# Performance work log

Measured on AMD Instinct MI355X. Metric: run time of the kernel, lower is better.

Reference implementation:

```python
import jax, jax.numpy as jnp
import numpy as np

N = 50000
E = 1600000
IN_CH = 128
HID = 32
HEADS = 4
OUT_CH = 64
NEG_SLOPE = 0.2


def _seg_softmax(e, seg, n):
    # e: [E,H], seg: [E] destination indices -> per-destination softmax
    m = jax.ops.segment_max(e, seg, num_segments=n)          # [N,H]
    ex = jnp.exp(e - m[seg])
    s = jax.ops.segment_sum(ex, seg, num_segments=n)         # [N,H]
    return ex / (s[seg] + 1e-16)


def _gat_conv(x, edge_index, W, a_src, a_dst, b, concat):
    # x: [N,Fin]; W: [Fin, H*C]; a_src/a_dst: [H,C]; b: [H*C] or [C]
    H, C = a_src.shape
    n = x.shape[0]
    h = (x @ W).reshape(n, H, C)                              # [N,H,C]
    src, dst = edge_index[0], edge_index[1]
    as_ = jnp.einsum('nhc,hc->nh', h, a_src)                  # [N,H]
    ad_ = jnp.einsum('nhc,hc->nh', h, a_dst)
    e = jax.nn.leaky_relu(as_[src] + ad_[dst], NEG_SLOPE)     # [E,H]
    alpha = _seg_softmax(e, dst, n)                           # [E,H]
    msg = h[src] * alpha[:, :, None]                          # [E,H,C]
    out = jax.ops.segment_sum(msg, dst, num_segments=n)       # [N,H,C]
    out = out.reshape(n, H * C) if concat else out.mean(axis=1)
    return out + b, alpha


def _layer_norm(x, w, b, eps=1e-5):
    mu = x.mean(-1, keepdims=True)
    var = x.var(-1, keepdims=True)
    return (x - mu) * jax.lax.rsqrt(var + eps) * w + b


def setup_inputs() -> dict:
    key = jax.random.key(0)
    ks = jax.random.split(key, 20)
    g = lambda k, s: jax.random.normal(k, s, dtype=jnp.float32) * 0.05
    d = {
        'x': jax.random.normal(ks[0], (N, IN_CH), dtype=jnp.float32),
        'edge_index': jax.random.randint(ks[1], (2, E), 0, N, dtype=jnp.int64),
        # gat1: in=IN_CH, out=HID, heads, concat
        'W1': g(ks[2], (IN_CH, HEADS * HID)),
        'a_src1': g(ks[3], (HEADS, HID)),
        'a_dst1': g(ks[4], (HEADS, HID)),
        'b1': jnp.zeros((HEADS * HID,), jnp.float32),
        'ln1_w': jnp.ones((HEADS * HID,), jnp.float32),
        'ln1_b': jnp.zeros((HEADS * HID,), jnp.float32),
        'Wskip': g(ks[5], (IN_CH, HEADS * HID)),
        'bskip': jnp.zeros((HEADS * HID,), jnp.float32),
        # gat2: in=HEADS*HID, out=HID, concat
        'W2': g(ks[6], (HEADS * HID, HEADS * HID)),
        'a_src2': g(ks[7], (HEADS, HID)),
        'a_dst2': g(ks[8], (HEADS, HID)),
        'b2': jnp.zeros((HEADS * HID,), jnp.float32),
        'ln2_w': jnp.ones((HEADS * HID,), jnp.float32),
        'ln2_b': jnp.zeros((HEADS * HID,), jnp.float32),
        # gat3: in=HEADS*HID, out=OUT_CH, concat=False (mean over heads)
        'W3': g(ks[9], (HEADS * HID, HEADS * OUT_CH)),
        'a_src3': g(ks[10], (HEADS, OUT_CH)),
        'a_dst3': g(ks[11], (HEADS, OUT_CH)),
        'b3': jnp.zeros((OUT_CH,), jnp.float32),
    }
    return d


def reference(x, edge_index, W1, a_src1, a_dst1, b1, ln1_w, ln1_b,
              Wskip, bskip, W2, a_src2, a_dst2, b2, ln2_w, ln2_b,
              W3, a_src3, a_dst3, b3):
    x_skip = x
    h, alpha1 = _gat_conv(x, edge_index, W1, a_src1, a_dst1, b1, concat=True)
    h = jax.nn.elu(h)
    h = _layer_norm(h, ln1_w, ln1_b)
    h = h + (x_skip @ Wskip + bskip)
    h, alpha2 = _gat_conv(h, edge_index, W2, a_src2, a_dst2, b2, concat=True)
    h = jax.nn.elu(h)
    h = _layer_norm(h, ln2_w, ln2_b)
    out, alpha3 = _gat_conv(h, edge_index, W3, a_src3, a_dst3, b3, concat=False)
    return out, alpha1, alpha2, alpha3
```

## Files before the change

kernel.cpp:

```cpp
#include <hip/hip_runtime.h>

#define NN 50000
#define EE 1600000
#define SCAN_B 196
#define NB 196
#define CHUNK 2048
#define G1 782
#define L1 (NB * G1)
#define B1 599

typedef __attribute__((ext_vector_type(8))) short bf16x8;
typedef __attribute__((ext_vector_type(4))) float f32x4;

__device__ __forceinline__ float bfu(unsigned short u) { return __uint_as_float((unsigned)u << 16); }
__device__ __forceinline__ float bflo(unsigned u) { return __uint_as_float(u << 16); }
__device__ __forceinline__ float bfhi(unsigned u) { return __uint_as_float(u & 0xffff0000u); }
__device__ __forceinline__ unsigned short f2bf(float f) {
    unsigned u = __float_as_uint(f);
    u += 0x7fff + ((u >> 16) & 1);
    return (unsigned short)(u >> 16);
}
__device__ __forceinline__ unsigned pk2(float a, float b) {
    return (unsigned)f2bf(a) | ((unsigned)f2bf(b) << 16);
}
__device__ __forceinline__ float cvt_load(const void* p, int i, bool f32) {
    if (f32) return ((const float*)p)[i];
    return bfu(((const unsigned short*)p)[i]);
}

__global__ void detect_k(const void* ei_raw, const void* x_raw, int* flags) {
    __shared__ int s_i64, s_f32;
    const int t = threadIdx.x;
    if (t == 0) { s_i64 = 1; s_f32 = 0; }
    __syncthreads();
    const int* ei32 = (const int*)ei_raw;
    if (ei32[2 * t + 1] != 0) atomicAnd(&s_i64, 0);
    const unsigned short* xu = (const unsigned short*)x_raw;
    int found = 0;
    for (int j = 0; j < 32; j++) {
        unsigned short u = xu[t * 32 + j];
        if ((u & 0x7F80) == 0x7F80) found = 1;
    }
    if (found) atomicOr(&s_f32, 1);
    __syncthreads();
    if (t == 0) { flags[0] = s_i64; flags[1] = s_f32; }
}

__global__ __launch_bounds__(256) void hist1_k(const void* ei_raw, const int* flags,
                                               int2* __restrict__ edges, int* __restrict__ cnt)
{
    __shared__ int h[NB];
    const int t = threadIdx.x;
    const int i64 = __builtin_amdgcn_readfirstlane(flags[0]);
    if (t < NB) h[t] = 0;
    __syncthreads();
    const int beg = blockIdx.x * CHUNK;
    const int end = min(beg + CHUNK, EE);
    for (int e = beg + t; e < end; e += 256) {
        int2 v;
        if (i64) { const long long* p = (const long long*)ei_raw; v.x = (int)p[e]; v.y = (int)p[EE + e]; }
        else     { const int* p = (const int*)ei_raw;             v.x = p[e];      v.y = p[EE + e];      }
        edges[e] = v;
        atomicAdd(&h[v.y >> 8], 1);
    }
    __syncthreads();
    if (t < NB) cnt[(size_t)t * G1 + blockIdx.x] = h[t];
}

__global__ __launch_bounds__(256) void scanAg_k(int* __restrict__ cnt, int* __restrict__ bsum2) {
    __shared__ int ps[256];
    const int b = blockIdx.x, t = threadIdx.x;
    const int i = b * 256 + t;
    const int v = (i < L1) ? cnt[i] : 0;
    ps[t] = v;
    __syncthreads();
    for (int off = 1; off < 256; off <<= 1) {
        const int u = (t >= off) ? ps[t - off] : 0;
        __syncthreads();
        ps[t] += u;
        __syncthreads();
    }
    if (i < L1) cnt[i] = ps[t] - v;
    if (t == 255) bsum2[b] = ps[255];
}
__global__ void scanBg_k(int* bsum2) {
    __shared__ int ps[256];
    const int t = threadIdx.x;
    int vals[3];
    int s = 0;
    #pragma unroll
    for (int i = 0; i < 3; i++) {
        const int idx = t * 3 + i;
        vals[i] = (idx < B1) ? bsum2[idx] : 0;
        s += vals[i];
    }
    ps[t] = s;
    __syncthreads();
    for (int off = 1; off < 256; off <<= 1) {
        const int u = (t >= off) ? ps[t - off] : 0;
        __syncthreads();
        ps[t] += u;
        __syncthreads();
    }
    int run = t ? ps[t - 1] : 0;
    #pragma unroll
    for (int i = 0; i < 3; i++) {
        const int idx = t * 3 + i;
        if (idx < B1) bsum2[idx] = run;
        run += vals[i];
    }
}
__global__ __launch_bounds__(256) void scanCg_k(int* __restrict__ cnt, const int* __restrict__ bsum2,
                                                int* __restrict__ bstart) {
    const int i = blockIdx.x * 256 + threadIdx.x;
    if (i < L1) {
        const int r = cnt[i] + bsum2[blockIdx.x];
        cnt[i] = r;
        if (i % G1 == 0) bstart[i / G1] = r;
    }
    if (i == 0) bstart[NB] = EE;
}

__global__ __launch_bounds__(256) void scatter_k(const int2* __restrict__ edges,
                                                 const int* __restrict__ cnt,
                                                 int2* __restrict__ bedges)
{
    __shared__ int ofs[NB];
    const int t = threadIdx.x;
    if (t < NB) ofs[t] = cnt[(size_t)t * G1 + blockIdx.x];
    __syncthreads();
    const int beg = blockIdx.x * CHUNK;
    const int end = min(beg + CHUNK, EE);
    for (int e = beg + t; e < end; e += 256) {
        const int2 v = edges[e];
        const int p = atomicAdd(&ofs[v.y >> 8], 1);
        bedges[p] = v;
    }
}

__global__ __launch_bounds__(256) void hist_k(const int2* __restrict__ bedges,
                                              const int* __restrict__ bstart, int* __restrict__ deg)
{
    __shared__ int h[256];
    const int b = blockIdx.x, t = threadIdx.x;
    h[t] = 0;
    __syncthreads();
    const int lo = bstart[b], hi = bstart[b + 1];
    for (int i = lo + t; i < hi; i += 256)
        atomicAdd(&h[bedges[i].y & 255], 1);
    __syncthreads();
    const int d = b * 256 + t;
    if (d < NN) deg[d] = h[t];
}

__global__ __launch_bounds__(256) void scanA_k(const int* __restrict__ deg,
                                               int* __restrict__ roff, int* __restrict__ bsum) {
    __shared__ int ps[256];
    const int b = blockIdx.x, t = threadIdx.x;
    const int i = b * 256 + t;
    const int v = (i < NN) ? deg[i] : 0;
    ps[t] = v;
    __syncthreads();
    for (int off = 1; off < 256; off <<= 1) {
        const int u = (t >= off) ? ps[t - off] : 0;
        __syncthreads();
        ps[t] += u;
        __syncthreads();
    }
    if (i < NN) roff[i] = ps[t] - v;
    if (t == 255) bsum[b] = ps[255];
}
__global__ void scanB_k(int* bsum) {
    __shared__ int ps[256];
    const int t = threadIdx.x;
    const int v = (t < SCAN_B) ? bsum[t] : 0;
    ps[t] = v;
    __syncthreads();
    for (int off = 1; off < 256; off <<= 1) {
        const int u = (t >= off) ? ps[t - off] : 0;
        __syncthreads();
        ps[t] += u;
        __syncthreads();
    }
    if (t < SCAN_B) bsum[t] = ps[t] - v;
}
__global__ __launch_bounds__(256) void scanC_k(int* __restrict__ roff, const int* __restrict__ bsum) {
    const int b = blockIdx.x, t = threadIdx.x;
    const int i = b * 256 + t;
    if (i < NN) roff[i] += bsum[b];
}

__global__ __launch_bounds__(256) void place_k(const int2* __restrict__ bedges,
                                               const int* __restrict__ bstart, const int* __restrict__ roff,
                                               int* __restrict__ csrc)
{
    __shared__ int cur[256];
    const int b = blockIdx.x, t = threadIdx.x;
    const int d = b * 256 + t;
    cur[t] = (d < NN) ? roff[d] : 0;
    __syncthreads();
    const int lo = bstart[b], hi = bstart[b + 1];
    for (int i = lo + t; i < hi; i += 256) {
        const int2 v = bedges[i];
        const int p = atomicAdd(&cur[v.y & 255], 1);
        csrc[p] = v.x;
    }
}

__global__ __launch_bounds__(256) void cvt_all_k(
    const void* x, const void* W1, const void* Wskip, const void* W2, const void* W3,
    const void* as1, const void* ad1, const void* b1, const void* l1w, const void* l1b,
    const void* bsk, const void* as2, const void* ad2, const void* b2, const void* l2w,
    const void* l2b, const void* as3, const void* ad3, const void* b3,
    unsigned short* xb, unsigned short* Wt1, unsigned short* Wts, unsigned short* Wt2,
    unsigned short* Wt3, float* smalls, const int* flags)
{
    const bool f32 = __builtin_amdgcn_readfirstlane(flags[1]) != 0;
    const int gid = blockIdx.x * 256 + threadIdx.x;
    if (gid < NN * 128) { xb[gid] = f2bf(cvt_load(x, gid, f32)); return; }
    int g = gid - NN * 128;
    if (g < 16384) { Wt1[g] = f2bf(cvt_load(W1,    (g & 127) * 128 + (g >> 7), f32)); return; }
    g -= 16384;
    if (g < 16384) { Wts[g] = f2bf(cvt_load(Wskip, (g & 127) * 128 + (g >> 7), f32)); return; }
    g -= 16384;
    if (g < 16384) { Wt2[g] = f2bf(cvt_load(W2,    (g & 127) * 128 + (g >> 7), f32)); return; }
    g -= 16384;
    if (g < 32768) { Wt3[g] = f2bf(cvt_load(W3,    (g & 127) * 256 + (g >> 7), f32)); return; }
    g -= 32768;
    if (g >= 2432) return;
    const void* src; int off;
    if      (g < 128)  { src = as1; off = g;        }
    else if (g < 256)  { src = ad1; off = g - 128;  }
    else if (g < 384)  { src = b1;  off = g - 256;  }
    else if (g < 512)  { src = l1w; off = g - 384;  }
    else if (g < 640)  { src = l1b; off = g - 512;  }
    else if (g < 768)  { src = bsk; off = g - 640;  }
    else if (g < 896)  { src = as2; off = g - 768;  }
    else if (g < 1024) { src = ad2; off = g - 896;  }
    else if (g < 1152) { src = b2;  off = g - 1024; }
    else if (g < 1280) { src = l2w; off = g - 1152; }
    else if (g < 1408) { src = l2b; off = g - 1280; }
    else if (g < 1664) { src = as3; off = g - 1408; }
    else if (g < 1920) { src = ad3; off = g - 1664; }
    else               { src = b3;  off = g - 1920; }
    smalls[g] = cvt_load(src, off, f32);
}

__global__ void prep_v_k(const unsigned short* __restrict__ Wt3, const float* __restrict__ as3,
                         const float* __restrict__ ad3, float* __restrict__ vsrc, float* __restrict__ vdst)
{
    const int t = blockIdx.x * 256 + threadIdx.x;
    if (t >= 512) return;
    const int h = t >> 7, k = t & 127;
    float ss = 0.f, dd = 0.f;
    for (int c = 0; c < 64; c++) {
        const float w = bfu(Wt3[(size_t)(h * 64 + c) * 128 + k]);
        ss = fmaf(w, as3[h * 64 + c], ss);
        dd = fmaf(w, ad3[h * 64 + c], dd);
    }
    vsrc[t] = ss; vdst[t] = dd;
}

template<int FOUT>
__global__ __launch_bounds__(256) void mfma_mm_k(
    const unsigned short* __restrict__ Xb, const unsigned short* __restrict__ Wt,
    unsigned short* __restrict__ Hb)
{
    constexpr int NT = FOUT / 16;
    const int tile = blockIdx.x * 4 + (threadIdx.x >> 6);
    if (tile >= 3125) return;
    const int l = threadIdx.x & 63;
    const int lr = l & 15, lq = l >> 4;
    const int m0 = tile * 16;
    f32x4 acc[NT];
    #pragma unroll
    for (int nt = 0; nt < NT; nt++) { acc[nt][0]=0.f; acc[nt][1]=0.f; acc[nt][2]=0.f; acc[nt][3]=0.f; }
    #pragma unroll
    for (int kb = 0; kb < 4; kb++) {
        const bf16x8 a = *(const bf16x8*)(Xb + (size_t)(m0 + lr) * 128 + kb * 32 + lq * 8);
        #pragma unroll
        for (int nt = 0; nt < NT; nt++) {
            const bf16x8 b = *(const bf16x8*)(Wt + (size_t)(nt * 16 + lr) * 128 + kb * 32 + lq * 8);
            acc[nt] = __builtin_amdgcn_mfma_f32_16x16x32_bf16(a, b, acc[nt], 0, 0, 0);
        }
    }
    #pragma unroll
    for (int nt = 0; nt < NT; nt++)
        #pragma unroll
        for (int r = 0; r < 4; r++)
            Hb[(size_t)(m0 + lq * 4 + r) * FOUT + nt * 16 + lr] = f2bf(acc[nt][r]);
}

__global__ __launch_bounds__(256) void mm12_k(
    const unsigned short* __restrict__ Xb, const unsigned short* __restrict__ Wt1,
    unsigned short* __restrict__ Hb, unsigned short* __restrict__ Sb)
{
    const int tile = blockIdx.x * 4 + (threadIdx.x >> 6);
    if (tile >= 3125) return;
    const int l = threadIdx.x & 63;
    const int lr = l & 15, lq = l >> 4;
    const int m0 = tile * 16;
    f32x4 acc[16];
    #pragma unroll
    for (int nt = 0; nt < 16; nt++) { acc[nt][0]=0.f; acc[nt][1]=0.f; acc[nt][2]=0.f; acc[nt][3]=0.f; }
    #pragma unroll
    for (int kb = 0; kb < 4; kb++) {
        const bf16x8 a = *(const bf16x8*)(Xb + (size_t)(m0 + lr) * 128 + kb * 32 + lq * 8);
        #pragma unroll
        for (int nt = 0; nt < 16; nt++) {
            const bf16x8 b = *(const bf16x8*)(Wt1 + (size_t)(nt * 16 + lr) * 128 + kb * 32 + lq * 8);
            acc[nt] = __builtin_amdgcn_mfma_f32_16x16x32_bf16(a, b, acc[nt], 0, 0, 0);
        }
    }
    #pragma unroll
    for (int nt = 0; nt < 8; nt++)
        #pragma unroll
        for (int r = 0; r < 4; r++)
            Hb[(size_t)(m0 + lq * 4 + r) * 128 + nt * 16 + lr] = f2bf(acc[nt][r]);
    #pragma unroll
    for (int nt = 8; nt < 16; nt++)
        #pragma unroll
        for (int r = 0; r < 4; r++)
            Sb[(size_t)(m0 + lq * 4 + r) * 128 + (nt - 8) * 16 + lr] = f2bf(acc[nt][r]);
}

__global__ __launch_bounds__(256) void dots_k(
    const unsigned short* __restrict__ Hb, const float* __restrict__ asrc,
    const float* __restrict__ adst, float* __restrict__ as_, float* __restrict__ dpk)
{
    const int node = blockIdx.x * 4 + (threadIdx.x >> 6);
    const int l = threadIdx.x & 63;
    const unsigned hv = *(const unsigned*)(Hb + (size_t)node * 128 + 2 * l);
    const float h0 = bfu((unsigned short)hv), h1 = bfu((unsigned short)(hv >> 16));
    const int hd = l >> 4;
    const int cc = (2 * l) & 31;
    float ps = h0 * asrc[hd * 32 + cc] + h1 * asrc[hd * 32 + cc + 1];
    float pd = h0 * adst[hd * 32 + cc] + h1 * adst[hd * 32 + cc + 1];
    #pragma unroll
    for (int m = 8; m; m >>= 1) { ps += __shfl_xor(ps, m); pd += __shfl_xor(pd, m); }
    if ((l & 15) == 0) {
        as_[(size_t)node * 4 + hd] = ps;
        dpk[(size_t)node * 8 + hd] = pd;
    }
}

__global__ __launch_bounds__(256) void dots3_k(
    const unsigned short* __restrict__ Xb, const float* __restrict__ vsrc,
    const float* __restrict__ vdst, float* __restrict__ as_, float* __restrict__ dpk)
{
    const int node = blockIdx.x * 4 + (threadIdx.x >> 6);
    const int l = threadIdx.x & 63;
    const unsigned hv = *(const unsigned*)(Xb + (size_t)node * 128 + 2 * l);
    const float x0 = bfu((unsigned short)hv), x1 = bfu((unsigned short)(hv >> 16));
    float s[4], d[4];
    #pragma unroll
    for (int h = 0; h < 4; h++) {
        s[h] = x0 * vsrc[h * 128 + 2 * l] + x1 * vsrc[h * 128 + 2 * l + 1];
        d[h] = x0 * vdst[h * 128 + 2 * l] + x1 * vdst[h * 128 + 2 * l + 1];
    }
    #pragma unroll
    for (int m = 32; m; m >>= 1)
        #pragma unroll
        for (int h = 0; h < 4; h++) { s[h] += __shfl_xor(s[h], m); d[h] += __shfl_xor(d[h], m); }
    if (l == 0) {
        #pragma unroll
        for (int h = 0; h < 4; h++) {
            as_[(size_t)node * 4 + h] = s[h];
            dpk[(size_t)node * 8 + h] = d[h];
        }
    }
}

__device__ __forceinline__ float4 edge_w(float4 as4, float4 ad4) {
    float4 e4;
    e4.x = as4.x + ad4.x; e4.y = as4.y + ad4.y; e4.z = as4.z + ad4.z; e4.w = as4.w + ad4.w;
    e4.x = e4.x >= 0.f ? e4.x : 0.2f * e4.x;
    e4.y = e4.y >= 0.f ? e4.y : 0.2f * e4.y;
    e4.z = e4.z >= 0.f ? e4.z : 0.2f * e4.z;
    e4.w = e4.w >= 0.f ? e4.w : 0.2f * e4.w;
    float4 w4;
    w4.x = __expf(e4.x); w4.y = __expf(e4.y); w4.z = __expf(e4.z); w4.w = __expf(e4.w);
    return w4;
}

template<bool HAS_SKIP>
__global__ __launch_bounds__(256) void fagg12_k(
    const int* __restrict__ roff, const int* __restrict__ deg,
    const int* __restrict__ csrc, const float* __restrict__ as_, float* __restrict__ dpk,
    const unsigned short* __restrict__ Hb,
    const float* __restrict__ b, const float* __restrict__ lnw, const float* __restrict__ lnb,
    const unsigned short* __restrict__ skipb, const float* __restrict__ bskip,
    unsigned short* __restrict__ xoutb)
{
    __shared__ float lws[4][512];
    const int warp = threadIdx.x >> 6;
    const int lane = threadIdx.x & 63;
    const int node = blockIdx.x * 4 + warp;
    const int q = lane & 15, g = lane >> 4;
    const int h = q >> 2;
    float* lw = lws[warp];
    const int ro = roff[node], dg = deg[node];
    const float4 ad4 = *(const float4*)(dpk + (size_t)node * 8);

    float4 sv = make_float4(0.f, 0.f, 0.f, 0.f);
    float acc[8];
    #pragma unroll
    for (int i = 0; i < 8; i++) acc[i] = 0.f;

    for (int j0 = 0; j0 < dg; j0 += 64) {
        const int jn = min(64, dg - j0);
        int src = 0;
        float4 w4 = make_float4(0.f, 0.f, 0.f, 0.f);
        if (lane < jn) {
            src = csrc[ro + j0 + lane];
            const float4 as4 = *(const float4*)(as_ + (size_t)src * 4);
            w4 = edge_w(as4, ad4);
            sv.x += w4.x; sv.y += w4.y; sv.z += w4.z; sv.w += w4.w;
        }
        const float sf = __int_as_float(src);
        *(float4*)(lw + lane * 8)     = make_float4(w4.x, sf, w4.y, sf);
        *(float4*)(lw + lane * 8 + 4) = make_float4(w4.z, sf, w4.w, sf);
        const int jq = (jn + 3) >> 2;
        #pragma unroll 2
        for (int j = 0; j < jq; j++) {
            const int e = 4 * j + g;
            const float2 rd = *(const float2*)(lw + e * 8 + h * 2);
            const float w = rd.x;
            const unsigned soff = (__float_as_uint(rd.y) << 8) + (unsigned)(q << 4);
            const uint4 hv = *(const uint4*)((const char*)Hb + soff);
            acc[0] = fmaf(w, bflo(hv.x), acc[0]);
            acc[1] = fmaf(w, bfhi(hv.x), acc[1]);
            acc[2] = fmaf(w, bflo(hv.y), acc[2]);
            acc[3] = fmaf(w, bfhi(hv.y), acc[3]);
            acc[4] = fmaf(w, bflo(hv.z), acc[4]);
            acc[5] = fmaf(w, bfhi(hv.z), acc[5]);
            acc[6] = fmaf(w, bflo(hv.w), acc[6]);
            acc[7] = fmaf(w, bfhi(hv.w), acc[7]);
        }
    }

    #pragma unroll
    for (int i = 0; i < 8; i++) {
        acc[i] += __shfl_xor(acc[i], 16);
        acc[i] += __shfl_xor(acc[i], 32);
    }
    #pragma unroll
    for (int m = 32; m; m >>= 1) {
        sv.x += __shfl_xor(sv.x, m); sv.y += __shfl_xor(sv.y, m);
        sv.z += __shfl_xor(sv.z, m); sv.w += __shfl_xor(sv.w, m);
    }
    float4 rs;
    rs.x = 1.f / (sv.x + 1e-16f); rs.y = 1.f / (sv.y + 1e-16f);
    rs.z = 1.f / (sv.z + 1e-16f); rs.w = 1.f / (sv.w + 1e-16f);
    if (lane == 0) *(float4*)(dpk + (size_t)node * 8 + 4) = rs;
    const float rsh = (h == 0) ? rs.x : (h == 1) ? rs.y : (h == 2) ? rs.z : rs.w;

    const float4 b0 = *(const float4*)(b + q * 8);
    const float4 b1 = *(const float4*)(b + q * 8 + 4);
    float v[8];
    v[0] = acc[0] * rsh + b0.x; v[1] = acc[1] * rsh + b0.y;
    v[2] = acc[2] * rsh + b0.z; v[3] = acc[3] * rsh + b0.w;
    v[4] = acc[4] * rsh + b1.x; v[5] = acc[5] * rsh + b1.y;
    v[6] = acc[6] * rsh + b1.z; v[7] = acc[7] * rsh + b1.w;
    float s1 = 0.f, s2 = 0.f;
    #pragma unroll
    for (int i = 0; i < 8; i++) {
        v[i] = v[i] > 0.f ? v[i] : expm1f(v[i]);
        s1 += v[i]; s2 += v[i] * v[i];
    }
    #pragma unroll
    for (int m = 8; m; m >>= 1) { s1 += __shfl_xor(s1, m); s2 += __shfl_xor(s2, m); }
    const float mu   = s1 * (1.f / 128.f);
    const float var  = s2 * (1.f / 128.f) - mu * mu;
    const float rstd = rsqrtf(var + 1e-5f);
    const float4 w0 = *(const float4*)(lnw + q * 8);
    const float4 w1 = *(const float4*)(lnw + q * 8 + 4);
    const float4 o0 = *(const float4*)(lnb + q * 8);
    const float4 o1 = *(const float4*)(lnb + q * 8 + 4);
    float y[8];
    y[0] = (v[0] - mu) * rstd * w0.x + o0.x; y[1] = (v[1] - mu) * rstd * w0.y + o0.y;
    y[2] = (v[2] - mu) * rstd * w0.z + o0.z; y[3] = (v[3] - mu) * rstd * w0.w + o0.w;
    y[4] = (v[4] - mu) * rstd * w1.x + o1.x; y[5] = (v[5] - mu) * rstd * w1.y + o1.y;
    y[6] = (v[6] - mu) * rstd * w1.z + o1.z; y[7] = (v[7] - mu) * rstd * w1.w + o1.w;
    if (HAS_SKIP) {
        const uint4 sk = *(const uint4*)(skipb + (size_t)node * 128 + q * 8);
        const float4 k0 = *(const float4*)(bskip + q * 8);
        const float4 k1 = *(const float4*)(bskip + q * 8 + 4);
        y[0] += bflo(sk.x) + k0.x; y[1] += bfhi(sk.x) + k0.y;
        y[2] += bflo(sk.y) + k0.z; y[3] += bfhi(sk.y) + k0.w;
        y[4] += bflo(sk.z) + k1.x; y[5] += bfhi(sk.z) + k1.y;
        y[6] += bflo(sk.w) + k1.z; y[7] += bfhi(sk.w) + k1.w;
    }
    if (g == 0) {
        uint4 pk;
        pk.x = pk2(y[0], y[1]); pk.y = pk2(y[2], y[3]);
        pk.z = pk2(y[4], y[5]); pk.w = pk2(y[6], y[7]);
        *(uint4*)(xoutb + (size_t)node * 128 + q * 8) = pk;
    }
}

__global__ __launch_bounds__(256) void fagg3_k(
    const int* __restrict__ roff, const int* __restrict__ deg,
    const int* __restrict__ csrc, const float* __restrict__ as_, float* __restrict__ dpk,
    const unsigned short* __restrict__ Xb,
    unsigned short* __restrict__ gout)
{
    __shared__ float lws[4][256];
    __shared__ int lss[4][64];
    const int warp = threadIdx.x >> 6;
    const int lane = threadIdx.x & 63;
    const int node = blockIdx.x * 4 + warp;
    const int q = lane & 31, g = lane >> 5;
    float* lw = lws[warp];
    int*   ls = lss[warp];
    const int ro = roff[node], dg = deg[node];
    const float4 ad4 = *(const float4*)(dpk + (size_t)node * 8);

    float4 sv = make_float4(0.f, 0.f, 0.f, 0.f);
    float acc[4][4];
    #pragma unroll
    for (int hh = 0; hh < 4; hh++)
        #pragma unroll
        for (int i = 0; i < 4; i++) acc[hh][i] = 0.f;

    for (int j0 = 0; j0 < dg; j0 += 64) {
        const int jn = min(64, dg - j0);
        int src = 0;
        float4 w4 = make_float4(0.f, 0.f, 0.f, 0.f);
        if (lane < jn) {
            src = csrc[ro + j0 + lane];
            const float4 as4 = *(const float4*)(as_ + (size_t)src * 4);
            w4 = edge_w(as4, ad4);
            sv.x += w4.x; sv.y += w4.y; sv.z += w4.z; sv.w += w4.w;
        }
        *(float4*)(lw + lane * 4) = w4;
        ls[lane] = src;
        const int jq = (jn + 1) >> 1;
        #pragma unroll 2
        for (int j = 0; j < jq; j++) {
            const int e = 2 * j + g;
            const float4 w = *(const float4*)(lw + e * 4);
            const int s_ = ls[e];
            const unsigned soff = ((unsigned)s_ << 8) + (unsigned)(q << 3);
            const uint2 hv = *(const uint2*)((const char*)Xb + soff);
            const float x0 = bflo(hv.x), x1 = bfhi(hv.x);
            const float x2 = bflo(hv.y), x3 = bfhi(hv.y);
            acc[0][0] = fmaf(w.x, x0, acc[0][0]); acc[0][1] = fmaf(w.x, x1, acc[0][1]);
            acc[0][2] = fmaf(w.x, x2, acc[0][2]); acc[0][3] = fmaf(w.x, x3, acc[0][3]);
            acc[1][0] = fmaf(w.y, x0, acc[1][0]); acc[1][1] = fmaf(w.y, x1, acc[1][1]);
            acc[1][2] = fmaf(w.y, x2, acc[1][2]); acc[1][3] = fmaf(w.y, x3, acc[1][3]);
            acc[2][0] = fmaf(w.z, x0, acc[2][0]); acc[2][1] = fmaf(w.z, x1, acc[2][1]);
            acc[2][2] = fmaf(w.z, x2, acc[2][2]); acc[2][3] = fmaf(w.z, x3, acc[2][3]);
            acc[3][0] = fmaf(w.w, x0, acc[3][0]); acc[3][1] = fmaf(w.w, x1, acc[3][1]);
            acc[3][2] = fmaf(w.w, x2, acc[3][2]); acc[3][3] = fmaf(w.w, x3, acc[3][3]);
        }
    }

    #pragma unroll
    for (int hh = 0; hh < 4; hh++)
        #pragma unroll
        for (int i = 0; i < 4; i++) acc[hh][i] += __shfl_xor(acc[hh][i], 32);
    #pragma unroll
    for (int m = 32; m; m >>= 1) {
        sv.x += __shfl_xor(sv.x, m); sv.y += __shfl_xor(sv.y, m);
        sv.z += __shfl_xor(sv.z, m); sv.w += __shfl_xor(sv.w, m);
    }
    float4 rs;
    rs.x = 1.f / (sv.x + 1e-16f); rs.y = 1.f / (sv.y + 1e-16f);
    rs.z = 1.f / (sv.z + 1e-16f); rs.w = 1.f / (sv.w + 1e-16f);
    if (lane == 0) *(float4*)(dpk + (size_t)node * 8 + 4) = rs;

    unsigned short* gr = gout + (size_t)node * 512 + 4 * q;
    if (g == 0) {
        uint2 p0, p1;
        p0.x = pk2(acc[0][0] * rs.x, acc[0][1] * rs.x);
        p0.y = pk2(acc[0][2] * rs.x, acc[0][3] * rs.x);
        p1.x = pk2(acc[1][0] * rs.y, acc[1][1] * rs.y);
        p1.y = pk2(acc[1][2] * rs.y, acc[1][3] * rs.y);
        *(uint2*)(gr)       = p0;
        *(uint2*)(gr + 128) = p1;
    } else {
        uint2 p2, p3;
        p2.x = pk2(acc[2][0] * rs.z, acc[2][1] * rs.z);
        p2.y = pk2(acc[2][2] * rs.z, acc[2][3] * rs.z);
        p3.x = pk2(acc[3][0] * rs.w, acc[3][1] * rs.w);
        p3.y = pk2(acc[3][2] * rs.w, acc[3][3] * rs.w);
        *(uint2*)(gr + 256) = p2;
        *(uint2*)(gr + 384) = p3;
    }
}

__global__ __launch_bounds__(256) void alpha_l_k(
    const int2* __restrict__ edges, const float* __restrict__ as_,
    const float* __restrict__ dpk, float* __restrict__ al)
{
    const int e = blockIdx.x * 256 + threadIdx.x;
    const int2 v = edges[e];
    const float4 as4 = *(const float4*)(as_ + (size_t)v.x * 4);
    const float4 ad4 = *(const float4*)(dpk + (size_t)v.y * 8);
    const float4 r   = *(const float4*)(dpk + (size_t)v.y * 8 + 4);
    const float4 w = edge_w(as4, ad4);
    float4 a; a.x = w.x * r.x; a.y = w.y * r.y; a.z = w.z * r.z; a.w = w.w * r.w;
    *(float4*)(al + (size_t)e * 4) = a;
}

__global__ __launch_bounds__(256) void proj3_k(
    const unsigned short* __restrict__ Gb, const unsigned short* __restrict__ Wt3,
    const float* __restrict__ b3, float* __restrict__ out)
{
    const int tile = blockIdx.x * 4 + (threadIdx.x >> 6);
    if (tile >= 3125) return;
    const int l = threadIdx.x & 63;
    const int lr = l & 15, lq = l >> 4;
    const int m0 = tile * 16;
    f32x4 acc[4];
    #pragma unroll
    for (int nt = 0; nt < 4; nt++) { acc[nt][0]=0.f; acc[nt][1]=0.f; acc[nt][2]=0.f; acc[nt][3]=0.f; }
    #pragma unroll
    for (int kb = 0; kb < 16; kb++) {
        const int h = kb >> 2;
        const int kk = (kb & 3) * 32 + lq * 8;
        const bf16x8 a = *(const bf16x8*)(Gb + (size_t)(m0 + lr) * 512 + kb * 32 + lq * 8);
        #pragma unroll
        for (int nt = 0; nt < 4; nt++) {
            const int c = nt * 16 + lr;
            const bf16x8 b = *(const bf16x8*)(Wt3 + (size_t)(h * 64 + c) * 128 + kk);
            acc[nt] = __builtin_amdgcn_mfma_f32_16x16x32_bf16(a, b, acc[nt], 0, 0, 0);
        }
    }
    #pragma unroll
    for (int nt = 0; nt < 4; nt++)
        #pragma unroll
        for (int r = 0; r < 4; r++) {
            const int col = nt * 16 + lr;
            out[(size_t)(m0 + lq * 4 + r) * 64 + col] = 0.25f * acc[nt][r] + b3[col];
        }
}

extern "C" void kernel_launch(void* const* d_in, const int* in_sizes, int n_in,
                              void* d_out, int out_size, void* d_ws, size_t ws_size,
                              hipStream_t stream)
{
    char* ws = (char*)d_ws;
    unsigned short* g_bf    = (unsigned short*)(ws);
    int2*           bedges  = (int2*)(ws);
    int*            csrc    = (int*)(ws + 51200000);
    unsigned short* x_bf    = (unsigned short*)(ws + 57600000);
    unsigned short* xcur_bf = (unsigned short*)(ws + 70400000);
    unsigned short* skip_bf = (unsigned short*)(ws + 83200000);
    unsigned short* Hbuf    = (unsigned short*)(ws + 96000000);
    int2*  edges  = (int2*)(ws + 108800000);
    float* as1b   = (float*)(ws + 121600000);
    float* as2b   = as1b + 200000;
    float* as3b   = as1b + 400000;
    float* dpk1   = as1b + 600000;
    float* dpk2   = as1b + 1000000;
    float* dpk3   = as1b + 1400000;
    int*   roff   = (int*)(ws + 128800000);
    int*   deg    = (int*)(ws + 129000000);
    int*   bsum   = (int*)(ws + 129200000);
    int*   flags  = (int*)(ws + 129402048);
    unsigned short* Wt1 = (unsigned short*)(ws + 129500000);
    unsigned short* Wts = Wt1 + 16384;
    unsigned short* Wt2 = Wts + 16384;
    unsigned short* Wt3 = Wt2 + 16384;
    float* smalls = (float*)(ws + 129700000);
    float* vsrc   = (float*)(ws + 129720000);
    float* vdst   = (float*)(ws + 129730000);
    int*   cnt    = (int*)(ws + 130000000);
    int*   bsum2  = (int*)(ws + 130700000);
    int*   bstart = (int*)(ws + 130710000);

    float* as1c = smalls;          float* ad1c = smalls + 128;
    float* b1c  = smalls + 256;    float* l1wc = smalls + 384;
    float* l1bc = smalls + 512;    float* bskc = smalls + 640;
    float* as2c = smalls + 768;    float* ad2c = smalls + 896;
    float* b2c  = smalls + 1024;   float* l2wc = smalls + 1152;
    float* l2bc = smalls + 1280;   float* as3c = smalls + 1408;
    float* ad3c = smalls + 1664;   float* b3c  = smalls + 1920;

    float* out = (float*)d_out;
    float* al1 = out + (size_t)NN * 64;
    float* al2 = al1 + (size_t)EE * 4;
    float* al3 = al2 + (size_t)EE * 4;

    detect_k<<<1, 256, 0, stream>>>(d_in[1], d_in[0], flags);
    hist1_k<<<G1, 256, 0, stream>>>(d_in[1], flags, edges, cnt);
    cvt_all_k<<<25330, 256, 0, stream>>>(
        d_in[0], d_in[2], d_in[8], d_in[10], d_in[16],
        d_in[3], d_in[4], d_in[5], d_in[6], d_in[7],
        d_in[9], d_in[11], d_in[12], d_in[13], d_in[14], d_in[15],
        d_in[17], d_in[18], d_in[19],
        x_bf, Wt1, Wts, Wt2, Wt3, smalls, flags);
    scanAg_k<<<B1, 256, 0, stream>>>(cnt, bsum2);
    scanBg_k<<<1, 256, 0, stream>>>(bsum2);
    scanCg_k<<<B1, 256, 0, stream>>>(cnt, bsum2, bstart);
    scatter_k<<<G1, 256, 0, stream>>>(edges, cnt, bedges);
    hist_k<<<NB, 256, 0, stream>>>(bedges, bstart, deg);
    scanA_k<<<SCAN_B, 256, 0, stream>>>(deg, roff, bsum);
    scanB_k<<<1, 256, 0, stream>>>(bsum);
    scanC_k<<<SCAN_B, 256, 0, stream>>>(roff, bsum);
    place_k<<<NB, 256, 0, stream>>>(bedges, bstart, roff, csrc);
    prep_v_k<<<2, 256, 0, stream>>>(Wt3, as3c, ad3c, vsrc, vdst);

    mm12_k<<<782, 256, 0, stream>>>(x_bf, Wt1, Hbuf, skip_bf);
    dots_k<<<12500, 256, 0, stream>>>(Hbuf, as1c, ad1c, as1b, dpk1);
    fagg12_k<true><<<12500, 256, 0, stream>>>(roff, deg, csrc, as1b, dpk1, Hbuf,
                                              b1c, l1wc, l1bc, skip_bf, bskc, xcur_bf);

    mfma_mm_k<128><<<782, 256, 0, stream>>>(xcur_bf, Wt2, Hbuf);
    dots_k<<<12500, 256, 0, stream>>>(Hbuf, as2c, ad2c, as2b, dpk2);
    fagg12_k<false><<<12500, 256, 0, stream>>>(roff, deg, csrc, as2b, dpk2, Hbuf,
                                               b2c, l2wc, l2bc, nullptr, nullptr, xcur_bf);

    dots3_k<<<12500, 256, 0, stream>>>(xcur_bf, vsrc, vdst, as3b, dpk3);
    fagg3_k<<<12500, 256, 0, stream>>>(roff, deg, csrc, as3b, dpk3, xcur_bf, g_bf);
    proj3_k<<<782, 256, 0, stream>>>(g_bf, Wt3, b3c, out);

    alpha_l_k<<<6250, 256, 0, stream>>>(edges, as1b, dpk1, al1);
    alpha_l_k<<<6250, 256, 0, stream>>>(edges, as2b, dpk2, al2);
    alpha_l_k<<<6250, 256, 0, stream>>>(edges, as3b, dpk3, al3);
}
```

Baseline: 605.2 us.

## Fuse attention dot products into matmul and aggregation epilogues; use packed FMA

Removes the separate dots_k and dots3_k launches. The per-node source and destination attention scores are now computed in the epilogues of the MFMA matmul kernels, and for layer 3 in the fagg12 layer-2 epilogue from the fp32 LayerNorm output. The aggregation inner loops also switch to 2-wide float vectors with elementwise fma, to encourage packed FMA instructions. This saves three kernel launches and three re-reads of the hidden features. The cost is extra shuffles and registers in the matmul and aggregation kernels, and layer-3 scores come from fp32 rather than bf16-rounded values.

Result: faster. 580.2 us (-4.1%).

```diff
diff --git a/kernel.cpp b/kernel.cpp
--- a/kernel.cpp
+++ b/kernel.cpp
@@ -11,10 +11,20 @@
 
 typedef __attribute__((ext_vector_type(8))) short bf16x8;
 typedef __attribute__((ext_vector_type(4))) float f32x4;
+typedef __attribute__((ext_vector_type(2))) float f32x2;
+
+#if __has_builtin(__builtin_elementwise_fma)
+#define PKFMA(a, b, c) __builtin_elementwise_fma((a), (b), (c))
+#else
+#define PKFMA(a, b, c) ((a) * (b) + (c))
+#endif
 
 __device__ __forceinline__ float bfu(unsigned short u) { return __uint_as_float((unsigned)u << 16); }
 __device__ __forceinline__ float bflo(unsigned u) { return __uint_as_float(u << 16); }
 __device__ __forceinline__ float bfhi(unsigned u) { return __uint_as_float(u & 0xffff0000u); }
+__device__ __forceinline__ f32x2 bfpk(unsigned u) {
+    f32x2 r; r.x = bflo(u); r.y = bfhi(u); return r;
+}
 __device__ __forceinline__ unsigned short f2bf(float f) {
     unsigned u = __float_as_uint(f);
     u += 0x7fff + ((u >> 16) & 1);
@@ -261,10 +271,12 @@
     vsrc[t] = ss; vdst[t] = dd;
 }
 
-template<int FOUT>
+template<int FOUT, bool DOTS>
 __global__ __launch_bounds__(256) void mfma_mm_k(
     const unsigned short* __restrict__ Xb, const unsigned short* __restrict__ Wt,
-    unsigned short* __restrict__ Hb)
+    unsigned short* __restrict__ Hb,
+    const float* __restrict__ asrc, const float* __restrict__ adst,
+    float* __restrict__ as_, float* __restrict__ dpk)
 {
     constexpr int NT = FOUT / 16;
     const int tile = blockIdx.x * 4 + (threadIdx.x >> 6);
@@ -289,11 +301,32 @@
         #pragma unroll
         for (int r = 0; r < 4; r++)
             Hb[(size_t)(m0 + lq * 4 + r) * FOUT + nt * 16 + lr] = f2bf(acc[nt][r]);
+    if (DOTS) {
+        #pragma unroll
+        for (int hd = 0; hd < 4; hd++) {
+            const float a0 = asrc[hd * 32 + lr], a1 = asrc[hd * 32 + 16 + lr];
+            const float d0 = adst[hd * 32 + lr], d1 = adst[hd * 32 + 16 + lr];
+            #pragma unroll
+            for (int r = 0; r < 4; r++) {
+                float ps = acc[2 * hd][r] * a0 + acc[2 * hd + 1][r] * a1;
+                float pd = acc[2 * hd][r] * d0 + acc[2 * hd + 1][r] * d1;
+                #pragma unroll
+                for (int m = 8; m; m >>= 1) { ps += __shfl_xor(ps, m); pd += __shfl_xor(pd, m); }
+                if (lr == 0) {
+                    const int node = m0 + lq * 4 + r;
+                    as_[(size_t)node * 4 + hd] = ps;
+                    dpk[(size_t)node * 8 + hd] = pd;
+                }
+            }
+        }
+    }
 }
 
 __global__ __launch_bounds__(256) void mm12_k(
     const unsigned short* __restrict__ Xb, const unsigned short* __restrict__ Wt1,
-    unsigned short* __restrict__ Hb, unsigned short* __restrict__ Sb)
+    unsigned short* __restrict__ Hb, unsigned short* __restrict__ Sb,
+    const float* __restrict__ asrc, const float* __restrict__ adst,
+    float* __restrict__ as_, float* __restrict__ dpk)
 {
     const int tile = blockIdx.x * 4 + (threadIdx.x >> 6);
     if (tile >= 3125) return;
@@ -322,51 +355,21 @@
         #pragma unroll
         for (int r = 0; r < 4; r++)
             Sb[(size_t)(m0 + lq * 4 + r) * 128 + (nt - 8) * 16 + lr] = f2bf(acc[nt][r]);
-}
-
-__global__ __launch_bounds__(256) void dots_k(
-    const unsigned short* __restrict__ Hb, const float* __restrict__ asrc,
-    const float* __restrict__ adst, float* __restrict__ as_, float* __restrict__ dpk)
-{
-    const int node = blockIdx.x * 4 + (threadIdx.x >> 6);
-    const int l = threadIdx.x & 63;
-    const unsigned hv = *(const unsigned*)(Hb + (size_t)node * 128 + 2 * l);
-    const float h0 = bfu((unsigned short)hv), h1 = bfu((unsigned short)(hv >> 16));
-    const int hd = l >> 4;
-    const int cc = (2 * l) & 31;
-    float ps = h0 * asrc[hd * 32 + cc] + h1 * asrc[hd * 32 + cc + 1];
-    float pd = h0 * adst[hd * 32 + cc] + h1 * adst[hd * 32 + cc + 1];
-    #pragma unroll
-    for (int m = 8; m; m >>= 1) { ps += __shfl_xor(ps, m); pd += __shfl_xor(pd, m); }
-    if ((l & 15) == 0) {
-        as_[(size_t)node * 4 + hd] = ps;
-        dpk[(size_t)node * 8 + hd] = pd;
-    }
-}
-
-__global__ __launch_bounds__(256) void dots3_k(
-    const unsigned short* __restrict__ Xb, const float* __restrict__ vsrc,
-    const float* __restrict__ vdst, float* __restrict__ as_, float* __restrict__ dpk)
-{
-    const int node = blockIdx.x * 4 + (threadIdx.x >> 6);
-    const int l = threadIdx.x & 63;
-    const unsigned hv = *(const unsigned*)(Xb + (size_t)node * 128 + 2 * l);
-    const float x0 = bfu((unsigned short)hv), x1 = bfu((unsigned short)(hv >> 16));
-    float s[4], d[4];
-    #pragma unroll
-    for (int h = 0; h < 4; h++) {
-        s[h] = x0 * vsrc[h * 128 + 2 * l] + x1 * vsrc[h * 128 + 2 * l + 1];
-        d[h] = x0 * vdst[h * 128 + 2 * l] + x1 * vdst[h * 128 + 2 * l + 1];
-    }
-    #pragma unroll
-    for (int m = 32; m; m >>= 1)
-        #pragma unroll
-        for (int h = 0; h < 4; h++) { s[h] += __shfl_xor(s[h], m); d[h] += __shfl_xor(d[h], m); }
-    if (l == 0) {
-        #pragma unroll
-        for (int h = 0; h < 4; h++) {
-            as_[(size_t)node * 4 + h] = s[h];
-            dpk[(size_t)node * 8 + h] = d[h];
+    #pragma unroll
+    for (int hd = 0; hd < 4; hd++) {
+        const float a0 = asrc[hd * 32 + lr], a1 = asrc[hd * 32 + 16 + lr];
+        const float d0 = adst[hd * 32 + lr], d1 = adst[hd * 32 + 16 + lr];
+        #pragma unroll
+        for (int r = 0; r < 4; r++) {
+            float ps = acc[2 * hd][r] * a0 + acc[2 * hd + 1][r] * a1;
+            float pd = acc[2 * hd][r] * d0 + acc[2 * hd + 1][r] * d1;
+            #pragma unroll
+            for (int m = 8; m; m >>= 1) { ps += __shfl_xor(ps, m); pd += __shfl_xor(pd, m); }
+            if (lr == 0) {
+                const int node = m0 + lq * 4 + r;
+                as_[(size_t)node * 4 + hd] = ps;
+                dpk[(size_t)node * 8 + hd] = pd;
+            }
         }
     }
 }
@@ -383,14 +386,16 @@
     return w4;
 }
 
-template<bool HAS_SKIP>
+template<bool HAS_SKIP, bool DOTS3>
 __global__ __launch_bounds__(256) void fagg12_k(
     const int* __restrict__ roff, const int* __restrict__ deg,
     const int* __restrict__ csrc, const float* __restrict__ as_, float* __restrict__ dpk,
     const unsigned short* __restrict__ Hb,
     const float* __restrict__ b, const float* __restrict__ lnw, const float* __restrict__ lnb,
     const unsigned short* __restrict__ skipb, const float* __restrict__ bskip,
-    unsigned short* __restrict__ xoutb)
+    unsigned short* __restrict__ xoutb,
+    const float* __restrict__ vsrc, const float* __restrict__ vdst,
+    float* __restrict__ as3o, float* __restrict__ dpk3o)
 {
     __shared__ float lws[4][512];
     const int warp = threadIdx.x >> 6;
@@ -403,9 +408,9 @@
     const float4 ad4 = *(const float4*)(dpk + (size_t)node * 8);
 
     float4 sv = make_float4(0.f, 0.f, 0.f, 0.f);
-    float acc[8];
-    #pragma unroll
-    for (int i = 0; i < 8; i++) acc[i] = 0.f;
+    f32x2 acc2[4];
+    #pragma unroll
+    for (int i = 0; i < 4; i++) { acc2[i].x = 0.f; acc2[i].y = 0.f; }
 
     for (int j0 = 0; j0 < dg; j0 += 64) {
         const int jn = min(64, dg - j0);
@@ -425,24 +430,22 @@
         for (int j = 0; j < jq; j++) {
             const int e = 4 * j + g;
             const float2 rd = *(const float2*)(lw + e * 8 + h * 2);
-            const float w = rd.x;
+            f32x2 ww; ww.x = rd.x; ww.y = rd.x;
             const unsigned soff = (__float_as_uint(rd.y) << 8) + (unsigned)(q << 4);
             const uint4 hv = *(const uint4*)((const char*)Hb + soff);
-            acc[0] = fmaf(w, bflo(hv.x), acc[0]);
-            acc[1] = fmaf(w, bfhi(hv.x), acc[1]);
-            acc[2] = fmaf(w, bflo(hv.y), acc[2]);
-            acc[3] = fmaf(w, bfhi(hv.y), acc[3]);
-            acc[4] = fmaf(w, bflo(hv.z), acc[4]);
-            acc[5] = fmaf(w, bfhi(hv.z), acc[5]);
-            acc[6] = fmaf(w, bflo(hv.w), acc[6]);
-            acc[7] = fmaf(w, bfhi(hv.w), acc[7]);
-        }
-    }
-
-    #pragma unroll
-    for (int i = 0; i < 8; i++) {
-        acc[i] += __shfl_xor(acc[i], 16);
-        acc[i] += __shfl_xor(acc[i], 32);
+            acc2[0] = PKFMA(ww, bfpk(hv.x), acc2[0]);
+            acc2[1] = PKFMA(ww, bfpk(hv.y), acc2[1]);
+            acc2[2] = PKFMA(ww, bfpk(hv.z), acc2[2]);
+            acc2[3] = PKFMA(ww, bfpk(hv.w), acc2[3]);
+        }
+    }
+
+    #pragma unroll
+    for (int i = 0; i < 4; i++) {
+        acc2[i].x += __shfl_xor(acc2[i].x, 16);
+        acc2[i].y += __shfl_xor(acc2[i].y, 16);
+        acc2[i].x += __shfl_xor(acc2[i].x, 32);
+        acc2[i].y += __shfl_xor(acc2[i].y, 32);
     }
     #pragma unroll
     for (int m = 32; m; m >>= 1) {
@@ -458,10 +461,10 @@
     const float4 b0 = *(const float4*)(b + q * 8);
     const float4 b1 = *(const float4*)(b + q * 8 + 4);
     float v[8];
-    v[0] = acc[0] * rsh + b0.x; v[1] = acc[1] * rsh + b0.y;
-    v[2] = acc[2] * rsh + b0.z; v[3] = acc[3] * rsh + b0.w;
-    v[4] = acc[4] * rsh + b1.x; v[5] = acc[5] * rsh + b1.y;
-    v[6] = acc[6] * rsh + b1.z; v[7] = acc[7] * rsh + b1.w;
+    v[0] = acc2[0].x * rsh + b0.x; v[1] = acc2[0].y * rsh + b0.y;
+    v[2] = acc2[1].x * rsh + b0.z; v[3] = acc2[1].y * rsh + b0.w;
+    v[4] = acc2[2].x * rsh + b1.x; v[5] = acc2[2].y * rsh + b1.y;
+    v[6] = acc2[3].x * rsh + b1.z; v[7] = acc2[3].y * rsh + b1.w;
     float s1 = 0.f, s2 = 0.f;
     #pragma unroll
     for (int i = 0; i < 8; i++) {
@@ -497,6 +500,25 @@
         pk.z = pk2(y[4], y[5]); pk.w = pk2(y[6], y[7]);
         *(uint4*)(xoutb + (size_t)node * 128 + q * 8) = pk;
     }
+    if (DOTS3) {
+        #pragma unroll
+        for (int hd = 0; hd < 4; hd++) {
+            const float4 vs0 = *(const float4*)(vsrc + hd * 128 + q * 8);
+            const float4 vs1 = *(const float4*)(vsrc + hd * 128 + q * 8 + 4);
+            const float4 vd0 = *(const float4*)(vdst + hd * 128 + q * 8);
+            const float4 vd1 = *(const float4*)(vdst + hd * 128 + q * 8 + 4);
+            float ss = y[0] * vs0.x + y[1] * vs0.y + y[2] * vs0.z + y[3] * vs0.w
+                     + y[4] * vs1.x + y[5] * vs1.y + y[6] * vs1.z + y[7] * vs1.w;
+            float dd = y[0] * vd0.x + y[1] * vd0.y + y[2] * vd0.z + y[3] * vd0.w
+                     + y[4] * vd1.x + y[5] * vd1.y + y[6] * vd1.z + y[7] * vd1.w;
+            #pragma unroll
+            for (int m = 8; m; m >>= 1) { ss += __shfl_xor(ss, m); dd += __shfl_xor(dd, m); }
+            if (lane == 0) {
+                as3o[(size_t)node * 4 + hd] = ss;
+                dpk3o[(size_t)node * 8 + hd] = dd;
+            }
+        }
+    }
 }
 
 __global__ __launch_bounds__(256) void fagg3_k(
@@ -517,11 +539,11 @@
     const float4 ad4 = *(const float4*)(dpk + (size_t)node * 8);
 
     float4 sv = make_float4(0.f, 0.f, 0.f, 0.f);
-    float acc[4][4];
+    f32x2 acc2[4][2];
     #pragma unroll
     for (int hh = 0; hh < 4; hh++)
         #pragma unroll
-        for (int i = 0; i < 4; i++) acc[hh][i] = 0.f;
+        for (int i = 0; i < 2; i++) { acc2[hh][i].x = 0.f; acc2[hh][i].y = 0.f; }
 
     for (int j0 = 0; j0 < dg; j0 += 64) {
         const int jn = min(64, dg - j0);
@@ -543,23 +565,25 @@
             const int s_ = ls[e];
             const unsigned soff = ((unsigned)s_ << 8) + (unsigned)(q << 3);
             const uint2 hv = *(const uint2*)((const char*)Xb + soff);
-            const float x0 = bflo(hv.x), x1 = bfhi(hv.x);
-            const float x2 = bflo(hv.y), x3 = bfhi(hv.y);
-            acc[0][0] = fmaf(w.x, x0, acc[0][0]); acc[0][1] = fmaf(w.x, x1, acc[0][1]);
-            acc[0][2] = fmaf(w.x, x2, acc[0][2]); acc[0][3] = fmaf(w.x, x3, acc[0][3]);
-            acc[1][0] = fmaf(w.y, x0, acc[1][0]); acc[1][1] = fmaf(w.y, x1, acc[1][1]);
-            acc[1][2] = fmaf(w.y, x2, acc[1][2]); acc[1][3] = fmaf(w.y, x3, acc[1][3]);
-            acc[2][0] = fmaf(w.z, x0, acc[2][0]); acc[2][1] = fmaf(w.z, x1, acc[2][1]);
-            acc[2][2] = fmaf(w.z, x2, acc[2][2]); acc[2][3] = fmaf(w.z, x3, acc[2][3]);
-            acc[3][0] = fmaf(w.w, x0, acc[3][0]); acc[3][1] = fmaf(w.w, x1, acc[3][1]);
-            acc[3][2] = fmaf(w.w, x2, acc[3][2]); acc[3][3] = fmaf(w.w, x3, acc[3][3]);
+            const f32x2 x01 = bfpk(hv.x), x23 = bfpk(hv.y);
+            f32x2 w0; w0.x = w.x; w0.y = w.x;
+            f32x2 w1; w1.x = w.y; w1.y = w.y;
+            f32x2 w2; w2.x = w.z; w2.y = w.z;
+            f32x2 w3; w3.x = w.w; w3.y = w.w;
+            acc2[0][0] = PKFMA(w0, x01, acc2[0][0]); acc2[0][1] = PKFMA(w0, x23, acc2[0][1]);
+            acc2[1][0] = PKFMA(w1, x01, acc2[1][0]); acc2[1][1] = PKFMA(w1, x23, acc2[1][1]);
+            acc2[2][0] = PKFMA(w2, x01, acc2[2][0]); acc2[2][1] = PKFMA(w2, x23, acc2[2][1]);
+            acc2[3][0] = PKFMA(w3, x01, acc2[3][0]); acc2[3][1] = PKFMA(w3, x23, acc2[3][1]);
         }
     }
 
     #pragma unroll
     for (int hh = 0; hh < 4; hh++)
         #pragma unroll
-        for (int i = 0; i < 4; i++) acc[hh][i] += __shfl_xor(acc[hh][i], 32);
+        for (int i = 0; i < 2; i++) {
+            acc2[hh][i].x += __shfl_xor(acc2[hh][i].x, 32);
+            acc2[hh][i].y += __shfl_xor(acc2[hh][i].y, 32);
+        }
     #pragma unroll
     for (int m = 32; m; m >>= 1) {
         sv.x += __shfl_xor(sv.x, m); sv.y += __shfl_xor(sv.y, m);
@@ -573,18 +597,18 @@
     unsigned short* gr = gout + (size_t)node * 512 + 4 * q;
     if (g == 0) {
         uint2 p0, p1;
-        p0.x = pk2(acc[0][0] * rs.x, acc[0][1] * rs.x);
-        p0.y = pk2(acc[0][2] * rs.x, acc[0][3] * rs.x);
-        p1.x = pk2(acc[1][0] * rs.y, acc[1][1] * rs.y);
-        p1.y = pk2(acc[1][2] * rs.y, acc[1][3] * rs.y);
+        p0.x = pk2(acc2[0][0].x * rs.x, acc2[0][0].y * rs.x);
+        p0.y = pk2(acc2[0][1].x * rs.x, acc2[0][1].y * rs.x);
+        p1.x = pk2(acc2[1][0].x * rs.y, acc2[1][0].y * rs.y);
+        p1.y = pk2(acc2[1][1].x * rs.y, acc2[1][1].y * rs.y);
         *(uint2*)(gr)       = p0;
         *(uint2*)(gr + 128) = p1;
     } else {
         uint2 p2, p3;
-        p2.x = pk2(acc[2][0] * rs.z, acc[2][1] * rs.z);
-        p2.y = pk2(acc[2][2] * rs.z, acc[2][3] * rs.z);
-        p3.x = pk2(acc[3][0] * rs.w, acc[3][1] * rs.w);
-        p3.y = pk2(acc[3][2] * rs.w, acc[3][3] * rs.w);
+        p2.x = pk2(acc2[2][0].x * rs.z, acc2[2][0].y * rs.z);
+        p2.y = pk2(acc2[2][1].x * rs.z, acc2[2][1].y * rs.z);
+        p3.x = pk2(acc2[3][0].x * rs.w, acc2[3][0].y * rs.w);
+        p3.y = pk2(acc2[3][1].x * rs.w, acc2[3][1].y * rs.w);
         *(uint2*)(gr + 256) = p2;
         *(uint2*)(gr + 384) = p3;
     }
@@ -703,17 +727,16 @@
     place_k<<<NB, 256, 0, stream>>>(bedges, bstart, roff, csrc);
     prep_v_k<<<2, 256, 0, stream>>>(Wt3, as3c, ad3c, vsrc, vdst);
 
-    mm12_k<<<782, 256, 0, stream>>>(x_bf, Wt1, Hbuf, skip_bf);
-    dots_k<<<12500, 256, 0, stream>>>(Hbuf, as1c, ad1c, as1b, dpk1);
-    fagg12_k<true><<<12500, 256, 0, stream>>>(roff, deg, csrc, as1b, dpk1, Hbuf,
-                                              b1c, l1wc, l1bc, skip_bf, bskc, xcur_bf);
-
-    mfma_mm_k<128><<<782, 256, 0, stream>>>(xcur_bf, Wt2, Hbuf);
-    dots_k<<<12500, 256, 0, stream>>>(Hbuf, as2c, ad2c, as2b, dpk2);
-    fagg12_k<false><<<12500, 256, 0, stream>>>(roff, deg, csrc, as2b, dpk2, Hbuf,
-                                               b2c, l2wc, l2bc, nullptr, nullptr, xcur_bf);
-
-    dots3_k<<<12500, 256, 0, stream>>>(xcur_bf, vsrc, vdst, as3b, dpk3);
+    mm12_k<<<782, 256, 0, stream>>>(x_bf, Wt1, Hbuf, skip_bf, as1c, ad1c, as1b, dpk1);
+    fagg12_k<true, false><<<12500, 256, 0, stream>>>(roff, deg, csrc, as1b, dpk1, Hbuf,
+                                                     b1c, l1wc, l1bc, skip_bf, bskc, xcur_bf,
+                                                     nullptr, nullptr, nullptr, nullptr);
+
+    mfma_mm_k<128, true><<<782, 256, 0, stream>>>(xcur_bf, Wt2, Hbuf, as2c, ad2c, as2b, dpk2);
+    fagg12_k<false, true><<<12500, 256, 0, stream>>>(roff, deg, csrc, as2b, dpk2, Hbuf,
+                                                     b2c, l2wc, l2bc, nullptr, nullptr, xcur_bf,
+                                                     vsrc, vdst, as3b, dpk3);
+
     fagg3_k<<<12500, 256, 0, stream>>>(roff, deg, csrc, as3b, dpk3, xcur_bf, g_bf);
     proj3_k<<<782, 256, 0, stream>>>(g_bf, Wt3, b3c, out);
 
```
